# Kernel tuning notes

Measured on AMD Instinct MI355X. Metric: run time of the kernel, lower is better.

## Reference

```python
import jax, jax.numpy as jnp
import numpy as np

B, S, D, E = 16, 2048, 1024, 1024
NEG = -1e13  # not_mask_sign from the original module


def setup_inputs() -> dict:
    key = jax.random.key(0)
    k1, k2, k3, k4, k5, k6 = jax.random.split(key, 6)
    return {
        "Q": jax.random.normal(k1, (B, S, D), dtype=jnp.float32),
        "K": jax.random.normal(k2, (B, S, D), dtype=jnp.float32),
        "V": jax.random.normal(k3, (B, S, D), dtype=jnp.float32),
        "pad_idxs": jax.random.randint(k4, (B,), 0, S, dtype=jnp.int64),
        "W": jax.random.normal(k5, (D, E), dtype=jnp.float32) * (1.0 / np.sqrt(D)),
        "b": jax.random.normal(k6, (E,), dtype=jnp.float32) * 0.01,
    }


def reference(Q, K, V, pad_idxs, W, b):
    d = Q.shape[2]
    # [B, S, S] attention scores
    scores = jnp.einsum("bqd,bkd->bqk", Q, K) / jnp.sqrt(jnp.asarray(d, Q.dtype))
    # Faithful to original: mask entries where row>=pad AND col>=pad
    idx = jnp.arange(scores.shape[1])
    p = pad_idxs[:, None, None]
    mask = (idx[None, :, None] >= p) & (idx[None, None, :] >= p)  # [B,S,S]
    scores = jnp.where(mask, jnp.asarray(NEG, scores.dtype), scores)
    attn = jax.nn.softmax(scores, axis=2)
    out = jnp.einsum("bqk,bkd->bqd", attn, V)
    return out @ W + b
```

## Files before the change

kernel.cpp:

```cpp
#include <hip/hip_runtime.h>

typedef unsigned short u16;
typedef unsigned int u32;
typedef long long ll;
typedef __attribute__((ext_vector_type(8))) short bf16x8;
typedef __attribute__((ext_vector_type(8))) unsigned short u16x8;
typedef __attribute__((ext_vector_type(4))) float f32x4;

__device__ __forceinline__ u16 f2bf(float f) {
  u32 x = __float_as_uint(f);
  x += 0x7fffu + ((x >> 16) & 1u);
  return (u16)(x >> 16);
}
__device__ __forceinline__ float bf2f(u16 u) {
  return __uint_as_float(((u32)u) << 16);
}

__device__ __forceinline__ int read_pad(const int* pw, int z) {
  int odd = pw[1] | pw[3] | pw[5] | pw[7] | pw[9] | pw[11] | pw[13] | pw[15];
  return (odd == 0) ? pw[2 * z] : pw[z];
}

__device__ __forceinline__ void stage_unit(const u16* gsrc, int gld, u16* dst,
                                           int ks, int wid, int lane) {
  const int rsub = lane >> 2;
  const int gk = ks * 32 + (((lane & 3) ^ ((lane >> 3) & 3)) * 8);
#pragma unroll
  for (int q = 0; q < 2; ++q) {
    const int r0 = (q * 8 + wid) * 16;
    __builtin_amdgcn_global_load_lds(
        (const __attribute__((address_space(1))) void*)(gsrc + (ll)(r0 + rsub) * gld + gk),
        (__attribute__((address_space(3))) void*)(dst + r0 * 32),
        16, 0, 0);
  }
}

template<int EPI>
__global__ __launch_bounds__(512, 2) void gemm8(
    const u16* __restrict__ A, const u16* __restrict__ B, void* __restrict__ C,
    int Kdim, int lda, int ldb, int ldc, ll sA, ll sB, ll sC,
    const float* __restrict__ bias, int NX, int NXY, int nwg) {
  __shared__ __align__(16) u16 ldsA[2][2 * 8192];
  __shared__ __align__(16) u16 ldsB[2][2 * 8192];

  const int orig = blockIdx.x;
  const int q8 = nwg >> 3, r8 = nwg & 7;
  const int xcd = orig & 7, inner = orig >> 3;
  const int wg = (xcd < r8 ? xcd * (q8 + 1) : r8 * (q8 + 1) + (xcd - r8) * q8) + inner;
  const int z = wg / NXY;
  const int rem = wg - z * NXY;
  const int by = rem / NX;
  const int bx = rem - by * NX;

  const int tid = threadIdx.x;
  const int wid = tid >> 6, lane = tid & 63;
  const int lr = lane & 15, lg = lane >> 4;
  const int wr = wid >> 2;
  const int wn64 = (wid & 3) * 64;
  const int bm = by * 256, bn = bx * 256;
  const u16* Ab = A + (ll)z * sA + (ll)bm * lda;
  const u16* Bb = B + (ll)z * sB + (ll)bn * ldb;

  const int aoff = lr * 32 + ((lg ^ ((lr >> 1) & 3)) * 8);

  f32x4 acc[8][4];
#pragma unroll
  for (int i = 0; i < 8; ++i)
#pragma unroll
    for (int j = 0; j < 4; ++j) acc[i][j] = (f32x4)0.0f;

#pragma unroll
  for (int p = 0; p < 4; ++p) {
    const int ks = p >> 1;
    if (p & 1) stage_unit(Bb, ldb, &ldsB[0][ks * 8192], ks, wid, lane);
    else       stage_unit(Ab, lda, &ldsA[0][ks * 8192], ks, wid, lane);
  }
  asm volatile("s_waitcnt vmcnt(4)" ::: "memory");
  __builtin_amdgcn_s_barrier();

  const int NT = Kdim >> 6;
  for (int t = 0; t < NT; ++t) {
    const int c = t & 1;
    u16* A_cur = &ldsA[c][0];
    u16* B_cur = &ldsB[c][0];
    u16* A_nxt = &ldsA[c ^ 1][0];
    u16* B_nxt = &ldsB[c ^ 1][0];
    const u16* Agn = Ab + (t + 1) * 64;
    const u16* Bgn = Bb + (t + 1) * 64;
    const bool stage = (t + 1 < NT);
    const bool last = (t + 1 == NT);
#pragma unroll
    for (int p = 0; p < 4; ++p) {
      const int ks = p >> 1, mh = p & 1;
      bf16x8 av[4], bv[4];
#pragma unroll
      for (int i = 0; i < 4; ++i) {
        av[i] = *(const bf16x8*)(A_cur + ks * 8192 +
                                 (wr * 128 + (mh * 4 + i) * 16) * 32 + aoff);
        bv[i] = *(const bf16x8*)(B_cur + ks * 8192 + (wn64 + i * 16) * 32 + aoff);
      }
      if (stage) {
        if (p & 1) stage_unit(Bgn, ldb, B_nxt + ks * 8192, ks, wid, lane);
        else       stage_unit(Agn, lda, A_nxt + ks * 8192, ks, wid, lane);
      }
      __builtin_amdgcn_s_barrier();
      asm volatile("s_waitcnt lgkmcnt(0)" ::: "memory");
      __builtin_amdgcn_sched_barrier(0);
      __builtin_amdgcn_s_setprio(1);
#pragma unroll
      for (int i = 0; i < 4; ++i)
#pragma unroll
        for (int j = 0; j < 4; ++j)
          acc[mh * 4 + i][j] = __builtin_amdgcn_mfma_f32_16x16x32_bf16(
              av[i], bv[j], acc[mh * 4 + i][j], 0, 0, 0);
      __builtin_amdgcn_s_setprio(0);
      if (p == 1) {
        if (last) asm volatile("s_waitcnt vmcnt(0)" ::: "memory");
        else      asm volatile("s_waitcnt vmcnt(4)" ::: "memory");
      } else if (p == 3) {
        if (!last) asm volatile("s_waitcnt vmcnt(4)" ::: "memory");
      }
      __builtin_amdgcn_s_barrier();
    }
  }

#pragma unroll
  for (int mf = 0; mf < 8; ++mf) {
    const int rowb = bm + wr * 128 + mf * 16 + 4 * lg;
#pragma unroll
    for (int nf = 0; nf < 4; ++nf) {
      const int col = bn + wn64 + nf * 16 + lr;
#pragma unroll
      for (int rg = 0; rg < 4; ++rg) {
        const int r = rowb + rg;
        if constexpr (EPI == 1) {
          ((u16*)C)[(ll)z * sC + (ll)r * ldc + col] = f2bf(acc[mf][nf][rg]);
        } else {
          ((float*)C)[(ll)z * sC + (ll)r * ldc + col] = acc[mf][nf][rg] + bias[col];
        }
      }
    }
  }
}

__global__ __launch_bounds__(256) void cvt_bf16(const float* __restrict__ src,
                                                u16* __restrict__ dst) {
  const ll i = ((ll)blockIdx.x * 256 + threadIdx.x) * 8;
  const float4 a = *(const float4*)(src + i);
  const float4 b = *(const float4*)(src + i + 4);
  u16x8 v;
  v[0] = f2bf(a.x); v[1] = f2bf(a.y); v[2] = f2bf(a.z); v[3] = f2bf(a.w);
  v[4] = f2bf(b.x); v[5] = f2bf(b.y); v[6] = f2bf(b.z); v[7] = f2bf(b.w);
  *(u16x8*)(dst + i) = v;
}

__global__ __launch_bounds__(256) void transpose_cvt(
    const float* __restrict__ src, u16* __restrict__ dst, int R, int C,
    ll sS, ll sD) {
  __shared__ u16 t[64][65];
  const int tid = threadIdx.x;
  const int r0 = blockIdx.y * 64, c0 = blockIdx.x * 64;
  const float* s = src + (ll)blockIdx.z * sS;
  u16* d = dst + (ll)blockIdx.z * sD;
#pragma unroll
  for (int it = 0; it < 16; ++it) {
    const int idx = it * 256 + tid;
    const int r = idx >> 6, c = idx & 63;
    t[r][c] = f2bf(s[(ll)(r0 + r) * C + c0 + c]);
  }
  __syncthreads();
#pragma unroll
  for (int it = 0; it < 16; ++it) {
    const int idx = it * 256 + tid;
    const int rr = idx >> 6, cc = idx & 63;
    d[(ll)(c0 + rr) * R + r0 + cc] = t[cc][rr];
  }
}

__global__ __launch_bounds__(256) void softmax_rows(u16* __restrict__ P,
                                                    const int* __restrict__ pad) {
  const int wid = threadIdx.x >> 6, lane = threadIdx.x & 63;
  const ll row = (ll)blockIdx.x * 4 + wid;
  const int z = (int)(row >> 11);
  const int r = (int)(row & 2047);
  const int p = read_pad(pad, z);
  const bool rmask = (r >= p);
  u16* ptr = P + row * 2048;
  float s[32];
#pragma unroll
  for (int i = 0; i < 4; ++i) {
    const u16x8 v = *(const u16x8*)(ptr + i * 512 + lane * 8);
#pragma unroll
    for (int j = 0; j < 8; ++j) {
      const int col = i * 512 + lane * 8 + j;
      float x = bf2f(v[j]) * 0.03125f;
      if (rmask && col >= p) x = -1e13f;
      s[i * 8 + j] = x;
    }
  }
  float m = s[0];
#pragma unroll
  for (int i = 1; i < 32; ++i) m = fmaxf(m, s[i]);
#pragma unroll
  for (int o = 1; o < 64; o <<= 1) m = fmaxf(m, __shfl_xor(m, o));
  float sum = 0.0f;
#pragma unroll
  for (int i = 0; i < 32; ++i) {
    s[i] = __expf(s[i] - m);
    sum += s[i];
  }
#pragma unroll
  for (int o = 1; o < 64; o <<= 1) sum += __shfl_xor(sum, o);
  const float inv = 1.0f / sum;
#pragma unroll
  for (int i = 0; i < 4; ++i) {
    u16x8 v;
#pragma unroll
    for (int j = 0; j < 8; ++j) v[j] = f2bf(s[i * 8 + j] * inv);
    *(u16x8*)(ptr + i * 512 + lane * 8) = v;
  }
}

__device__ __forceinline__ void stage_f32(const float* src, ll base, int ld,
                                          u16* lds, int tid) {
#pragma unroll
  for (int p = 0; p < 4; ++p) {
    int chunk = p * 256 + tid;
    int r = chunk >> 3, slot = chunk & 7;
    const float* s = src + base + (ll)r * ld + slot * 8;
    const float4 a = *(const float4*)s;
    const float4 b = *(const float4*)(s + 4);
    u16x8 v;
    v[0] = f2bf(a.x); v[1] = f2bf(a.y); v[2] = f2bf(a.z); v[3] = f2bf(a.w);
    v[4] = f2bf(b.x); v[5] = f2bf(b.y); v[6] = f2bf(b.z); v[7] = f2bf(b.w);
    *(u16x8*)(lds + r * 64 + (slot ^ (r & 7)) * 8) = v;
  }
}

__global__ __launch_bounds__(256) void gemm_f32in(
    const float* __restrict__ A, const float* __restrict__ B,
    u16* __restrict__ C, int Kdim, int lda, int ldb, int ldc,
    ll sA, ll sB, ll sC) {
  __shared__ __align__(16) u16 As[128 * 64];
  __shared__ __align__(16) u16 Bs[128 * 64];
  const int tid = threadIdx.x;
  const int z = blockIdx.z;
  const int bm = blockIdx.y * 128, bn = blockIdx.x * 128;
  const ll abase = (ll)z * sA + (ll)bm * lda;
  const ll bbase = (ll)z * sB + (ll)bn * ldb;
  const int wid = tid >> 6, lane = tid & 63;
  const int wm = (wid >> 1) * 64, wn = (wid & 1) * 64;
  const int lr = lane & 15, lg = lane >> 4;

  f32x4 acc[4][4];
#pragma unroll
  for (int i = 0; i < 4; ++i)
#pragma unroll
    for (int j = 0; j < 4; ++j) acc[i][j] = (f32x4)0.0f;

  for (int k0 = 0; k0 < Kdim; k0 += 64) {
    __syncthreads();
    stage_f32(A, abase + k0, lda, As, tid);
    stage_f32(B, bbase + k0, ldb, Bs, tid);
    __syncthreads();
#pragma unroll
    for (int kk = 0; kk < 2; ++kk) {
      bf16x8 av[4], bv[4];
#pragma unroll
      for (int i = 0; i < 4; ++i) {
        const int ra = wm + i * 16 + lr;
        av[i] = *(const bf16x8*)(As + ra * 64 + (((kk * 4 + lg) ^ (ra & 7)) * 8));
        const int rb = wn + i * 16 + lr;
        bv[i] = *(const bf16x8*)(Bs + rb * 64 + (((kk * 4 + lg) ^ (rb & 7)) * 8));
      }
#pragma unroll
      for (int i = 0; i < 4; ++i)
#pragma unroll
        for (int j = 0; j < 4; ++j)
          acc[i][j] = __builtin_amdgcn_mfma_f32_16x16x32_bf16(av[i], bv[j],
                                                              acc[i][j], 0, 0, 0);
    }
  }
#pragma unroll
  for (int i = 0; i < 4; ++i) {
    const int rowb = bm + wm + i * 16 + 4 * lg;
#pragma unroll
    for (int j = 0; j < 4; ++j) {
      const int col = bn + wn + j * 16 + lr;
#pragma unroll
      for (int rg = 0; rg < 4; ++rg)
        C[(ll)z * sC + (ll)(rowb + rg) * ldc + col] = f2bf(acc[i][j][rg]);
    }
  }
}

extern "C" void kernel_launch(void* const* d_in, const int* in_sizes, int n_in,
                              void* d_out, int out_size, void* d_ws,
                              size_t ws_size, hipStream_t stream) {
  const float* Q = (const float*)d_in[0];
  const float* Km = (const float*)d_in[1];
  const float* V = (const float*)d_in[2];
  const int* pad = (const int*)d_in[3];
  const float* W = (const float*)d_in[4];
  const float* bias = (const float*)d_in[5];
  float* out = (float*)d_out;

  const int B = 16, S = 2048, D = 1024, E = 1024;
  const ll SS = (ll)S * S, SD = (ll)S * D;

  u16* P = (u16*)d_out;
  char* ws = (char*)d_ws;

  const size_t MB64 = (size_t)B * S * D * 2;
  const size_t szWt = (size_t)D * E * 2;

  if (ws_size >= 3 * MB64 + szWt) {
    u16* Qb = (u16*)ws;
    u16* Kb = (u16*)(ws + MB64);
    u16* Vt = (u16*)(ws + 2 * MB64);
    u16* Wt = (u16*)(ws + 3 * MB64);
    u16* X = Qb;

    const int nv = (int)(((ll)B * S * D) / (8 * 256));
    cvt_bf16<<<nv, 256, 0, stream>>>(Q, Qb);
    cvt_bf16<<<nv, 256, 0, stream>>>(Km, Kb);
    transpose_cvt<<<dim3(D / 64, S / 64, B), 256, 0, stream>>>(V, Vt, S, D, SD, SD);
    transpose_cvt<<<dim3(E / 64, D / 64, 1), 256, 0, stream>>>(W, Wt, D, E, 0, 0);

    gemm8<1><<<dim3(1024), 512, 0, stream>>>(
        Qb, Kb, P, D, D, D, S, SD, SD, SS, nullptr, 8, 64, 1024);
    softmax_rows<<<dim3(B * S / 4), 256, 0, stream>>>(P, pad);
    gemm8<1><<<dim3(512), 512, 0, stream>>>(
        P, Vt, X, S, S, S, D, SS, SD, SD, nullptr, 4, 32, 512);
    gemm8<2><<<dim3(512), 512, 0, stream>>>(
        X, Wt, out, D, D, D, E, 0, 0, 0, bias, 4, 512, 512);
  } else if (ws_size >= 2 * MB64 + szWt) {
    u16* Vt = (u16*)ws;
    u16* Wt = (u16*)(ws + MB64);
    u16* X = (u16*)(ws + MB64 + szWt);

    transpose_cvt<<<dim3(D / 64, S / 64, B), 256, 0, stream>>>(V, Vt, S, D, SD, SD);
    transpose_cvt<<<dim3(E / 64, D / 64, 1), 256, 0, stream>>>(W, Wt, D, E, 0, 0);
    gemm_f32in<<<dim3(S / 128, S / 128, B), 256, 0, stream>>>(
        Q, Km, P, D, D, D, S, SD, SD, SS);
    softmax_rows<<<dim3(B * S / 4), 256, 0, stream>>>(P, pad);
    gemm8<1><<<dim3(512), 512, 0, stream>>>(
        P, Vt, X, S, S, S, D, SS, SD, SD, nullptr, 4, 32, 512);
    gemm8<2><<<dim3(512), 512, 0, stream>>>(
        X, Wt, out, D, D, D, E, 0, 0, 0, bias, 4, 512, 512);
  } else {
    u16* Wt = (u16*)ws;
    u16* Vtb = (u16*)(ws + szWt);
    u16* X = (u16*)(ws + szWt + (size_t)D * S * 2);

    transpose_cvt<<<dim3(E / 64, D / 64, 1), 256, 0, stream>>>(W, Wt, D, E, 0, 0);
    gemm_f32in<<<dim3(S / 128, S / 128, B), 256, 0, stream>>>(
        Q, Km, P, D, D, D, S, SD, SD, SS);
    softmax_rows<<<dim3(B * S / 4), 256, 0, stream>>>(P, pad);
    for (int b = 0; b < B; ++b) {
      transpose_cvt<<<dim3(D / 64, S / 64, 1), 256, 0, stream>>>(
          V + (ll)b * SD, Vtb, S, D, 0, 0);
      gemm8<1><<<dim3(32), 512, 0, stream>>>(
          P + (ll)b * SS, Vtb, X + (ll)b * SD, S, S, S, D, 0, 0, 0, nullptr,
          4, 32, 32);
    }
    gemm8<2><<<dim3(512), 512, 0, stream>>>(
        X, Wt, out, D, D, D, E, 0, 0, 0, bias, 4, 512, 512);
  }
}
```

Before: 560.1 us.

## Restructure GEMM inner loop to reuse B fragments and fuse scale/mask into QK epilogue

The GEMM main loop now iterates over two k-steps instead of four phases. It loads B fragments once per k-step and reuses them across both M halves, and it drops the explicit lgkmcnt wait and sched_barrier. A new epilogue variant for the QK^T GEMM applies the 1/sqrt(d) scale and the pad mask before the bf16 store, so the softmax kernel skips both on the main path. The aim is fewer LDS reads and less softmax ALU work. Removing the explicit LDS wait leaves ordering to the compiler, and the interleaving of A and B staging changes.

```diff
diff --git a/kernel.cpp b/kernel.cpp
--- a/kernel.cpp
+++ b/kernel.cpp
@@ -39,7 +39,8 @@
 __global__ __launch_bounds__(512, 2) void gemm8(
     const u16* __restrict__ A, const u16* __restrict__ B, void* __restrict__ C,
     int Kdim, int lda, int ldb, int ldc, ll sA, ll sB, ll sC,
-    const float* __restrict__ bias, int NX, int NXY, int nwg) {
+    const int* __restrict__ pad, const float* __restrict__ bias,
+    int NX, int NXY, int nwg) {
   __shared__ __align__(16) u16 ldsA[2][2 * 8192];
   __shared__ __align__(16) u16 ldsB[2][2 * 8192];
 
@@ -90,40 +91,50 @@
     const bool stage = (t + 1 < NT);
     const bool last = (t + 1 == NT);
 #pragma unroll
-    for (int p = 0; p < 4; ++p) {
-      const int ks = p >> 1, mh = p & 1;
+    for (int ks = 0; ks < 2; ++ks) {
       bf16x8 av[4], bv[4];
 #pragma unroll
       for (int i = 0; i < 4; ++i) {
+        bv[i] = *(const bf16x8*)(B_cur + ks * 8192 + (wn64 + i * 16) * 32 + aoff);
+        av[i] = *(const bf16x8*)(A_cur + ks * 8192 + (wr * 128 + i * 16) * 32 + aoff);
+      }
+      if (stage) stage_unit(Agn, lda, A_nxt + ks * 8192, ks, wid, lane);
+      __builtin_amdgcn_s_barrier();
+      __builtin_amdgcn_s_setprio(1);
+#pragma unroll
+      for (int i = 0; i < 4; ++i)
+#pragma unroll
+        for (int j = 0; j < 4; ++j)
+          acc[i][j] = __builtin_amdgcn_mfma_f32_16x16x32_bf16(
+              av[i], bv[j], acc[i][j], 0, 0, 0);
+      __builtin_amdgcn_s_setprio(0);
+      __builtin_amdgcn_s_barrier();
+#pragma unroll
+      for (int i = 0; i < 4; ++i)
         av[i] = *(const bf16x8*)(A_cur + ks * 8192 +
-                                 (wr * 128 + (mh * 4 + i) * 16) * 32 + aoff);
-        bv[i] = *(const bf16x8*)(B_cur + ks * 8192 + (wn64 + i * 16) * 32 + aoff);
-      }
-      if (stage) {
-        if (p & 1) stage_unit(Bgn, ldb, B_nxt + ks * 8192, ks, wid, lane);
-        else       stage_unit(Agn, lda, A_nxt + ks * 8192, ks, wid, lane);
-      }
+                                 (wr * 128 + (4 + i) * 16) * 32 + aoff);
+      if (stage) stage_unit(Bgn, ldb, B_nxt + ks * 8192, ks, wid, lane);
       __builtin_amdgcn_s_barrier();
-      asm volatile("s_waitcnt lgkmcnt(0)" ::: "memory");
-      __builtin_amdgcn_sched_barrier(0);
       __builtin_amdgcn_s_setprio(1);
 #pragma unroll
       for (int i = 0; i < 4; ++i)
 #pragma unroll
         for (int j = 0; j < 4; ++j)
-          acc[mh * 4 + i][j] = __builtin_amdgcn_mfma_f32_16x16x32_bf16(
-              av[i], bv[j], acc[mh * 4 + i][j], 0, 0, 0);
+          acc[4 + i][j] = __builtin_amdgcn_mfma_f32_16x16x32_bf16(
+              av[i], bv[j], acc[4 + i][j], 0, 0, 0);
       __builtin_amdgcn_s_setprio(0);
-      if (p == 1) {
+      if (ks == 0) {
         if (last) asm volatile("s_waitcnt vmcnt(0)" ::: "memory");
         else      asm volatile("s_waitcnt vmcnt(4)" ::: "memory");
-      } else if (p == 3) {
-        if (!last) asm volatile("s_waitcnt vmcnt(4)" ::: "memory");
+      } else if (!last) {
+        asm volatile("s_waitcnt vmcnt(4)" ::: "memory");
       }
       __builtin_amdgcn_s_barrier();
     }
   }
 
+  int p = 0;
+  if constexpr (EPI == 0) p = read_pad(pad, z);
 #pragma unroll
   for (int mf = 0; mf < 8; ++mf) {
     const int rowb = bm + wr * 128 + mf * 16 + 4 * lg;
@@ -133,7 +144,11 @@
 #pragma unroll
       for (int rg = 0; rg < 4; ++rg) {
         const int r = rowb + rg;
-        if constexpr (EPI == 1) {
+        if constexpr (EPI == 0) {
+          float v = acc[mf][nf][rg] * 0.03125f;
+          if (r >= p && col >= p) v = -1e13f;
+          ((u16*)C)[(ll)z * sC + (ll)r * ldc + col] = f2bf(v);
+        } else if constexpr (EPI == 1) {
           ((u16*)C)[(ll)z * sC + (ll)r * ldc + col] = f2bf(acc[mf][nf][rg]);
         } else {
           ((float*)C)[(ll)z * sC + (ll)r * ldc + col] = acc[mf][nf][rg] + bias[col];
@@ -177,14 +192,19 @@
   }
 }
 
+template<bool MASKED>
 __global__ __launch_bounds__(256) void softmax_rows(u16* __restrict__ P,
                                                     const int* __restrict__ pad) {
   const int wid = threadIdx.x >> 6, lane = threadIdx.x & 63;
   const ll row = (ll)blockIdx.x * 4 + wid;
   const int z = (int)(row >> 11);
   const int r = (int)(row & 2047);
-  const int p = read_pad(pad, z);
-  const bool rmask = (r >= p);
+  int p = 0;
+  bool rmask = false;
+  if constexpr (MASKED) {
+    p = read_pad(pad, z);
+    rmask = (r >= p);
+  }
   u16* ptr = P + row * 2048;
   float s[32];
 #pragma unroll
@@ -192,9 +212,12 @@
     const u16x8 v = *(const u16x8*)(ptr + i * 512 + lane * 8);
 #pragma unroll
     for (int j = 0; j < 8; ++j) {
-      const int col = i * 512 + lane * 8 + j;
-      float x = bf2f(v[j]) * 0.03125f;
-      if (rmask && col >= p) x = -1e13f;
+      float x = bf2f(v[j]);
+      if constexpr (MASKED) {
+        const int col = i * 512 + lane * 8 + j;
+        x *= 0.03125f;
+        if (rmask && col >= p) x = -1e13f;
+      }
       s[i * 8 + j] = x;
     }
   }
@@ -327,13 +350,13 @@
     transpose_cvt<<<dim3(D / 64, S / 64, B), 256, 0, stream>>>(V, Vt, S, D, SD, SD);
     transpose_cvt<<<dim3(E / 64, D / 64, 1), 256, 0, stream>>>(W, Wt, D, E, 0, 0);
 
-    gemm8<1><<<dim3(1024), 512, 0, stream>>>(
-        Qb, Kb, P, D, D, D, S, SD, SD, SS, nullptr, 8, 64, 1024);
-    softmax_rows<<<dim3(B * S / 4), 256, 0, stream>>>(P, pad);
+    gemm8<0><<<dim3(1024), 512, 0, stream>>>(
+        Qb, Kb, P, D, D, D, S, SD, SD, SS, pad, nullptr, 8, 64, 1024);
+    softmax_rows<false><<<dim3(B * S / 4), 256, 0, stream>>>(P, pad);
     gemm8<1><<<dim3(512), 512, 0, stream>>>(
-        P, Vt, X, S, S, S, D, SS, SD, SD, nullptr, 4, 32, 512);
+        P, Vt, X, S, S, S, D, SS, SD, SD, nullptr, nullptr, 4, 32, 512);
     gemm8<2><<<dim3(512), 512, 0, stream>>>(
-        X, Wt, out, D, D, D, E, 0, 0, 0, bias, 4, 512, 512);
+        X, Wt, out, D, D, D, E, 0, 0, 0, nullptr, bias, 4, 512, 512);
   } else if (ws_size >= 2 * MB64 + szWt) {
     u16* Vt = (u16*)ws;
     u16* Wt = (u16*)(ws + MB64);
@@ -343,11 +366,11 @@
     transpose_cvt<<<dim3(E / 64, D / 64, 1), 256, 0, stream>>>(W, Wt, D, E, 0, 0);
     gemm_f32in<<<dim3(S / 128, S / 128, B), 256, 0, stream>>>(
         Q, Km, P, D, D, D, S, SD, SD, SS);
-    softmax_rows<<<dim3(B * S / 4), 256, 0, stream>>>(P, pad);
+    softmax_rows<true><<<dim3(B * S / 4), 256, 0, stream>>>(P, pad);
     gemm8<1><<<dim3(512), 512, 0, stream>>>(
-        P, Vt, X, S, S, S, D, SS, SD, SD, nullptr, 4, 32, 512);
+        P, Vt, X, S, S, S, D, SS, SD, SD, nullptr, nullptr, 4, 32, 512);
     gemm8<2><<<dim3(512), 512, 0, stream>>>(
-        X, Wt, out, D, D, D, E, 0, 0, 0, bias, 4, 512, 512);
+        X, Wt, out, D, D, D, E, 0, 0, 0, nullptr, bias, 4, 512, 512);
   } else {
     u16* Wt = (u16*)ws;
     u16* Vtb = (u16*)(ws + szWt);
@@ -356,15 +379,15 @@
     transpose_cvt<<<dim3(E / 64, D / 64, 1), 256, 0, stream>>>(W, Wt, D, E, 0, 0);
     gemm_f32in<<<dim3(S / 128, S / 128, B), 256, 0, stream>>>(
         Q, Km, P, D, D, D, S, SD, SD, SS);
-    softmax_rows<<<dim3(B * S / 4), 256, 0, stream>>>(P, pad);
+    softmax_rows<true><<<dim3(B * S / 4), 256, 0, stream>>>(P, pad);
     for (int b = 0; b < B; ++b) {
       transpose_cvt<<<dim3(D / 64, S / 64, 1), 256, 0, stream>>>(
           V + (ll)b * SD, Vtb, S, D, 0, 0);
       gemm8<1><<<dim3(32), 512, 0, stream>>>(
           P + (ll)b * SS, Vtb, X + (ll)b * SD, S, S, S, D, 0, 0, 0, nullptr,
-          4, 32, 32);
+          nullptr, 4, 32, 32);
     }
     gemm8<2><<<dim3(512), 512, 0, stream>>>(
-        X, Wt, out, D, D, D, E, 0, 0, 0, bias, 4, 512, 512);
-  }
-}
+        X, Wt, out, D, D, D, E, 0, 0, 0, nullptr, bias, 4, 512, 512);
+  }
+}
```

New measurement: 525.8 us. 6.1% less time.

## Fuse softmax exponent into QK GEMM epilogue and defer normalization to PV

Applied to the files above, without the earlier changes.

Removes the separate softmax pass. The QK GEMM epilogue now applies the scale, the pad mask and the exp directly, with no max subtraction. It writes unnormalized bf16 probabilities and accumulates row sums into a workspace buffer with atomics. The PV GEMM epilogue divides by those row sums. The GEMM tile is also changed to 256x128 with a K-step of 32, a simpler single-stage-ahead pipeline and a higher occupancy target. Skipping the max subtraction risks overflow for large scores, and the shallower K-step adds barrier and wait overhead per iteration.

```diff
diff --git a/kernel.cpp b/kernel.cpp
--- a/kernel.cpp
+++ b/kernel.cpp
@@ -21,12 +21,13 @@
   return (odd == 0) ? pw[2 * z] : pw[z];
 }
 
+template<int ROWS>
 __device__ __forceinline__ void stage_unit(const u16* gsrc, int gld, u16* dst,
-                                           int ks, int wid, int lane) {
+                                           int wid, int lane) {
   const int rsub = lane >> 2;
-  const int gk = ks * 32 + (((lane & 3) ^ ((lane >> 3) & 3)) * 8);
-#pragma unroll
-  for (int q = 0; q < 2; ++q) {
+  const int gk = ((lane & 3) ^ ((lane >> 3) & 3)) * 8;
+#pragma unroll
+  for (int q = 0; q < ROWS / 128; ++q) {
     const int r0 = (q * 8 + wid) * 16;
     __builtin_amdgcn_global_load_lds(
         (const __attribute__((address_space(1))) void*)(gsrc + (ll)(r0 + rsub) * gld + gk),
@@ -36,12 +37,13 @@
 }
 
 template<int EPI>
-__global__ __launch_bounds__(512, 2) void gemm8(
+__global__ __launch_bounds__(512, 4) void gemm8(
     const u16* __restrict__ A, const u16* __restrict__ B, void* __restrict__ C,
     int Kdim, int lda, int ldb, int ldc, ll sA, ll sB, ll sC,
-    const float* __restrict__ bias, int NX, int NXY, int nwg) {
-  __shared__ __align__(16) u16 ldsA[2][2 * 8192];
-  __shared__ __align__(16) u16 ldsB[2][2 * 8192];
+    const int* __restrict__ pad, const float* __restrict__ bias,
+    float* __restrict__ lsum, int NX, int NXY, int nwg) {
+  __shared__ __align__(16) u16 ldsA[2][256 * 32];
+  __shared__ __align__(16) u16 ldsB[2][128 * 32];
 
   const int orig = blockIdx.x;
   const int q8 = nwg >> 3, r8 = nwg & 7;
@@ -56,91 +58,111 @@
   const int wid = tid >> 6, lane = tid & 63;
   const int lr = lane & 15, lg = lane >> 4;
   const int wr = wid >> 2;
-  const int wn64 = (wid & 3) * 64;
-  const int bm = by * 256, bn = bx * 256;
+  const int wn32 = (wid & 3) * 32;
+  const int bm = by * 256, bn = bx * 128;
   const u16* Ab = A + (ll)z * sA + (ll)bm * lda;
   const u16* Bb = B + (ll)z * sB + (ll)bn * ldb;
 
   const int aoff = lr * 32 + ((lg ^ ((lr >> 1) & 3)) * 8);
 
-  f32x4 acc[8][4];
+  f32x4 acc[8][2];
 #pragma unroll
   for (int i = 0; i < 8; ++i)
 #pragma unroll
-    for (int j = 0; j < 4; ++j) acc[i][j] = (f32x4)0.0f;
-
-#pragma unroll
-  for (int p = 0; p < 4; ++p) {
-    const int ks = p >> 1;
-    if (p & 1) stage_unit(Bb, ldb, &ldsB[0][ks * 8192], ks, wid, lane);
-    else       stage_unit(Ab, lda, &ldsA[0][ks * 8192], ks, wid, lane);
-  }
-  asm volatile("s_waitcnt vmcnt(4)" ::: "memory");
+    for (int j = 0; j < 2; ++j) acc[i][j] = (f32x4)0.0f;
+
+  const int NT = Kdim >> 5;
+
+  stage_unit<256>(Ab, lda, &ldsA[0][0], wid, lane);
+  stage_unit<128>(Bb, ldb, &ldsB[0][0], wid, lane);
+  asm volatile("s_waitcnt vmcnt(0)" ::: "memory");
   __builtin_amdgcn_s_barrier();
 
-  const int NT = Kdim >> 6;
   for (int t = 0; t < NT; ++t) {
     const int c = t & 1;
-    u16* A_cur = &ldsA[c][0];
-    u16* B_cur = &ldsB[c][0];
-    u16* A_nxt = &ldsA[c ^ 1][0];
-    u16* B_nxt = &ldsB[c ^ 1][0];
-    const u16* Agn = Ab + (t + 1) * 64;
-    const u16* Bgn = Bb + (t + 1) * 64;
-    const bool stage = (t + 1 < NT);
-    const bool last = (t + 1 == NT);
-#pragma unroll
-    for (int p = 0; p < 4; ++p) {
-      const int ks = p >> 1, mh = p & 1;
-      bf16x8 av[4], bv[4];
-#pragma unroll
-      for (int i = 0; i < 4; ++i) {
-        av[i] = *(const bf16x8*)(A_cur + ks * 8192 +
-                                 (wr * 128 + (mh * 4 + i) * 16) * 32 + aoff);
-        bv[i] = *(const bf16x8*)(B_cur + ks * 8192 + (wn64 + i * 16) * 32 + aoff);
-      }
-      if (stage) {
-        if (p & 1) stage_unit(Bgn, ldb, B_nxt + ks * 8192, ks, wid, lane);
-        else       stage_unit(Agn, lda, A_nxt + ks * 8192, ks, wid, lane);
-      }
-      __builtin_amdgcn_s_barrier();
-      asm volatile("s_waitcnt lgkmcnt(0)" ::: "memory");
-      __builtin_amdgcn_sched_barrier(0);
-      __builtin_amdgcn_s_setprio(1);
-#pragma unroll
-      for (int i = 0; i < 4; ++i)
-#pragma unroll
-        for (int j = 0; j < 4; ++j)
-          acc[mh * 4 + i][j] = __builtin_amdgcn_mfma_f32_16x16x32_bf16(
-              av[i], bv[j], acc[mh * 4 + i][j], 0, 0, 0);
-      __builtin_amdgcn_s_setprio(0);
-      if (p == 1) {
-        if (last) asm volatile("s_waitcnt vmcnt(0)" ::: "memory");
-        else      asm volatile("s_waitcnt vmcnt(4)" ::: "memory");
-      } else if (p == 3) {
-        if (!last) asm volatile("s_waitcnt vmcnt(4)" ::: "memory");
-      }
-      __builtin_amdgcn_s_barrier();
-    }
-  }
-
+    if (t + 1 < NT) {
+      stage_unit<256>(Ab + (ll)(t + 1) * 32, lda, &ldsA[c ^ 1][0], wid, lane);
+      stage_unit<128>(Bb + (ll)(t + 1) * 32, ldb, &ldsB[c ^ 1][0], wid, lane);
+    }
+    bf16x8 bv[2], av[4];
+#pragma unroll
+    for (int i = 0; i < 2; ++i)
+      bv[i] = *(const bf16x8*)(&ldsB[c][0] + (wn32 + i * 16) * 32 + aoff);
+#pragma unroll
+    for (int i = 0; i < 4; ++i)
+      av[i] = *(const bf16x8*)(&ldsA[c][0] + (wr * 128 + i * 16) * 32 + aoff);
+    __builtin_amdgcn_s_setprio(1);
+#pragma unroll
+    for (int i = 0; i < 4; ++i)
+#pragma unroll
+      for (int j = 0; j < 2; ++j)
+        acc[i][j] = __builtin_amdgcn_mfma_f32_16x16x32_bf16(av[i], bv[j],
+                                                            acc[i][j], 0, 0, 0);
+    __builtin_amdgcn_s_setprio(0);
+#pragma unroll
+    for (int i = 0; i < 4; ++i)
+      av[i] = *(const bf16x8*)(&ldsA[c][0] + (wr * 128 + (4 + i) * 16) * 32 + aoff);
+    __builtin_amdgcn_s_setprio(1);
+#pragma unroll
+    for (int i = 0; i < 4; ++i)
+#pragma unroll
+      for (int j = 0; j < 2; ++j)
+        acc[4 + i][j] = __builtin_amdgcn_mfma_f32_16x16x32_bf16(
+            av[i], bv[j], acc[4 + i][j], 0, 0, 0);
+    __builtin_amdgcn_s_setprio(0);
+    asm volatile("s_waitcnt vmcnt(0)" ::: "memory");
+    __builtin_amdgcn_s_barrier();
+  }
+
+  int p = 0;
+  if constexpr (EPI == 0) p = read_pad(pad, z);
 #pragma unroll
   for (int mf = 0; mf < 8; ++mf) {
-    const int rowb = bm + wr * 128 + mf * 16 + 4 * lg;
-#pragma unroll
-    for (int nf = 0; nf < 4; ++nf) {
-      const int col = bn + wn64 + nf * 16 + lr;
-#pragma unroll
-      for (int rg = 0; rg < 4; ++rg) {
-        const int r = rowb + rg;
-        if constexpr (EPI == 1) {
-          ((u16*)C)[(ll)z * sC + (ll)r * ldc + col] = f2bf(acc[mf][nf][rg]);
-        } else {
-          ((float*)C)[(ll)z * sC + (ll)r * ldc + col] = acc[mf][nf][rg] + bias[col];
+#pragma unroll
+    for (int rg = 0; rg < 4; ++rg) {
+      const int row = bm + wr * 128 + mf * 16 + 4 * lg + rg;
+      if constexpr (EPI == 0) {
+        float part = 0.0f;
+#pragma unroll
+        for (int nf = 0; nf < 2; ++nf) {
+          const int col = bn + wn32 + nf * 16 + lr;
+          float e;
+          if (row >= p && col >= p) e = (p == 0) ? 1.0f : 0.0f;
+          else e = __expf(acc[mf][nf][rg] * 0.03125f);
+          part += e;
+          ((u16*)C)[(ll)z * sC + (ll)row * ldc + col] = f2bf(e);
+        }
+        part += __shfl_xor(part, 1);
+        part += __shfl_xor(part, 2);
+        part += __shfl_xor(part, 4);
+        part += __shfl_xor(part, 8);
+        if (lr == 0) atomicAdd(&lsum[z * 2048 + row], part);
+      } else if constexpr (EPI == 3) {
+        const float linv = 1.0f / lsum[z * 2048 + row];
+#pragma unroll
+        for (int nf = 0; nf < 2; ++nf) {
+          const int col = bn + wn32 + nf * 16 + lr;
+          ((u16*)C)[(ll)z * sC + (ll)row * ldc + col] =
+              f2bf(acc[mf][nf][rg] * linv);
+        }
+      } else {
+#pragma unroll
+        for (int nf = 0; nf < 2; ++nf) {
+          const int col = bn + wn32 + nf * 16 + lr;
+          if constexpr (EPI == 1) {
+            ((u16*)C)[(ll)z * sC + (ll)row * ldc + col] = f2bf(acc[mf][nf][rg]);
+          } else {
+            ((float*)C)[(ll)z * sC + (ll)row * ldc + col] =
+                acc[mf][nf][rg] + bias[col];
+          }
         }
       }
     }
   }
+}
+
+__global__ __launch_bounds__(256) void zerof(float* __restrict__ p) {
+  p[blockIdx.x * 256 + threadIdx.x] = 0.0f;
 }
 
 __global__ __launch_bounds__(256) void cvt_bf16(const float* __restrict__ src,
@@ -313,27 +335,29 @@
 
   const size_t MB64 = (size_t)B * S * D * 2;
   const size_t szWt = (size_t)D * E * 2;
-
-  if (ws_size >= 3 * MB64 + szWt) {
+  const size_t szL = (size_t)B * S * 4;
+
+  if (ws_size >= 3 * MB64 + szWt + szL) {
     u16* Qb = (u16*)ws;
     u16* Kb = (u16*)(ws + MB64);
     u16* Vt = (u16*)(ws + 2 * MB64);
     u16* Wt = (u16*)(ws + 3 * MB64);
+    float* lsum = (float*)(ws + 3 * MB64 + szWt);
     u16* X = Qb;
 
     const int nv = (int)(((ll)B * S * D) / (8 * 256));
+    zerof<<<dim3(B * S / 256), 256, 0, stream>>>(lsum);
     cvt_bf16<<<nv, 256, 0, stream>>>(Q, Qb);
     cvt_bf16<<<nv, 256, 0, stream>>>(Km, Kb);
     transpose_cvt<<<dim3(D / 64, S / 64, B), 256, 0, stream>>>(V, Vt, S, D, SD, SD);
     transpose_cvt<<<dim3(E / 64, D / 64, 1), 256, 0, stream>>>(W, Wt, D, E, 0, 0);
 
-    gemm8<1><<<dim3(1024), 512, 0, stream>>>(
-        Qb, Kb, P, D, D, D, S, SD, SD, SS, nullptr, 8, 64, 1024);
-    softmax_rows<<<dim3(B * S / 4), 256, 0, stream>>>(P, pad);
-    gemm8<1><<<dim3(512), 512, 0, stream>>>(
-        P, Vt, X, S, S, S, D, SS, SD, SD, nullptr, 4, 32, 512);
-    gemm8<2><<<dim3(512), 512, 0, stream>>>(
-        X, Wt, out, D, D, D, E, 0, 0, 0, bias, 4, 512, 512);
+    gemm8<0><<<dim3(2048), 512, 0, stream>>>(
+        Qb, Kb, P, D, D, D, S, SD, SD, SS, pad, nullptr, lsum, 16, 128, 2048);
+    gemm8<3><<<dim3(1024), 512, 0, stream>>>(
+        P, Vt, X, S, S, S, D, SS, SD, SD, nullptr, nullptr, lsum, 8, 64, 1024);
+    gemm8<2><<<dim3(1024), 512, 0, stream>>>(
+        X, Wt, out, D, D, D, E, 0, 0, 0, nullptr, bias, nullptr, 8, 1024, 1024);
   } else if (ws_size >= 2 * MB64 + szWt) {
     u16* Vt = (u16*)ws;
     u16* Wt = (u16*)(ws + MB64);
@@ -344,10 +368,10 @@
     gemm_f32in<<<dim3(S / 128, S / 128, B), 256, 0, stream>>>(
         Q, Km, P, D, D, D, S, SD, SD, SS);
     softmax_rows<<<dim3(B * S / 4), 256, 0, stream>>>(P, pad);
-    gemm8<1><<<dim3(512), 512, 0, stream>>>(
-        P, Vt, X, S, S, S, D, SS, SD, SD, nullptr, 4, 32, 512);
-    gemm8<2><<<dim3(512), 512, 0, stream>>>(
-        X, Wt, out, D, D, D, E, 0, 0, 0, bias, 4, 512, 512);
+    gemm8<1><<<dim3(1024), 512, 0, stream>>>(
+        P, Vt, X, S, S, S, D, SS, SD, SD, nullptr, nullptr, nullptr, 8, 64, 1024);
+    gemm8<2><<<dim3(1024), 512, 0, stream>>>(
+        X, Wt, out, D, D, D, E, 0, 0, 0, nullptr, bias, nullptr, 8, 1024, 1024);
   } else {
     u16* Wt = (u16*)ws;
     u16* Vtb = (u16*)(ws + szWt);
@@ -360,11 +384,11 @@
     for (int b = 0; b < B; ++b) {
       transpose_cvt<<<dim3(D / 64, S / 64, 1), 256, 0, stream>>>(
           V + (ll)b * SD, Vtb, S, D, 0, 0);
-      gemm8<1><<<dim3(32), 512, 0, stream>>>(
+      gemm8<1><<<dim3(64), 512, 0, stream>>>(
           P + (ll)b * SS, Vtb, X + (ll)b * SD, S, S, S, D, 0, 0, 0, nullptr,
-          4, 32, 32);
-    }
-    gemm8<2><<<dim3(512), 512, 0, stream>>>(
-        X, Wt, out, D, D, D, E, 0, 0, 0, bias, 4, 512, 512);
-  }
-}
+          nullptr, nullptr, 8, 64, 64);
+    }
+    gemm8<2><<<dim3(1024), 512, 0, stream>>>(
+        X, Wt, out, D, D, D, E, 0, 0, 0, nullptr, bias, nullptr, 8, 1024, 1024);
+  }
+}
```

After: 640.9 us. 14.4% more time.
